# Kernel tuning notes

Hardware: AMD Instinct MI355X
Metric: run time of the kernel (lower is better)

## Reference

```python
import jax, jax.numpy as jnp
import numpy as np
from jax.scipy.special import erf

F = 64          # scalar feature channels (hidden_irreps multiplicity)
S = 9           # spherical harmonics dim for max_ell=2
NB = 8          # num_bessel
RMAX = 5.0
PPOLY = 5       # num_polynomial_cutoff
AVG_NEIGH = 16.0
SIGMA = 1.0     # atomic_multipoles_smearing_width
KE = 1.0        # Coulomb constant (model units)
N = 20000; G = 20; E = 320000; NEL = 10; L = 2; HMLP = 16

def _sph_l2(u):
    # real spherical harmonics up to l=2, e3nn 'component' normalization,
    # with permute_to_e3nn_convention (y, z, x) ordering for l=1
    x, y, z = u[..., 0], u[..., 1], u[..., 2]
    s3 = 1.7320508075688772; s5 = 2.23606797749979; s15 = 3.872983346207417
    return jnp.stack([jnp.ones_like(x),
                      s3 * y, s3 * z, s3 * x,
                      s15 * x * y, s15 * y * z, 0.5 * s5 * (3.0 * z * z - 1.0),
                      s15 * x * z, 0.5 * s15 * (x * x - y * y)], axis=-1)

def _radial(r):
    # Bessel basis with smooth polynomial cutoff (p = PPOLY)
    n = jnp.arange(1, NB + 1, dtype=r.dtype)
    rb = jnp.sqrt(2.0 / RMAX) * jnp.sin(n * jnp.pi * r[:, None] / RMAX) / r[:, None]
    x = r / RMAX
    p = float(PPOLY)
    u = (1.0 - 0.5 * (p + 1.0) * (p + 2.0) * x**PPOLY
         + p * (p + 2.0) * x**(PPOLY + 1) - 0.5 * p * (p + 1.0) * x**(PPOLY + 2))
    u = jnp.where(x < 1.0, u, 0.0)
    return rb * u[:, None]

def setup_inputs() -> dict:
    key = jax.random.key(0)
    ks = jax.random.split(key, 20)
    Ng = N // G
    species = jax.random.randint(ks[0], (N,), 0, NEL)
    node_attrs = jax.nn.one_hot(species, NEL, dtype=jnp.float32)
    positions = jax.random.uniform(ks[1], (N, 3), dtype=jnp.float32) * 10.0
    g = jax.random.randint(ks[2], (E,), 0, G)
    s_loc = jax.random.randint(ks[3], (E,), 0, Ng)
    off = jax.random.randint(ks[4], (E,), 1, Ng)   # avoid self edges
    r_loc = (s_loc + off) % Ng
    edge_index = jnp.stack([g * Ng + s_loc, g * Ng + r_loc], axis=0)
    batch = jnp.repeat(jnp.arange(G), Ng)
    sc = 0.1
    atomic_energies = jax.random.normal(ks[5], (NEL,)) * sc
    embed_w = jax.random.normal(ks[6], (NEL, F)) * sc
    radial_w1 = jax.random.normal(ks[7], (L, NB, 64)) * 0.3
    radial_b1 = jnp.zeros((L, 64), jnp.float32)
    radial_w2 = jax.random.normal(ks[8], (L, 64, F)) * 0.2
    prod_w = jax.random.normal(ks[9], (L, NEL, F)) * 0.3
    readout_w = jax.random.normal(ks[10], (L, F)) * sc
    ro2_w1 = jax.random.normal(ks[11], (F, HMLP)) * 0.2
    ro2_b1 = jnp.zeros((HMLP,), jnp.float32)
    ro2_w2 = jax.random.normal(ks[12], (HMLP, 1)) * 0.2
    charge_w = jax.random.normal(ks[13], (L, F)) * sc
    flux_w = jax.random.normal(ks[14], (L, NB)) * sc
    formal_charges = jax.random.normal(ks[15], (NEL,)) * 0.5
    return dict(node_attrs=node_attrs, positions=positions, edge_index=edge_index,
                batch=batch, num_graphs=G, atomic_energies=atomic_energies,
                embed_w=embed_w, radial_w1=radial_w1, radial_b1=radial_b1,
                radial_w2=radial_w2, prod_w=prod_w, readout_w=readout_w,
                ro2_w1=ro2_w1, ro2_b1=ro2_b1, ro2_w2=ro2_w2,
                charge_w=charge_w, flux_w=flux_w, formal_charges=formal_charges)

def reference(node_attrs, positions, edge_index, batch, num_graphs,
              atomic_energies, embed_w, radial_w1, radial_b1, radial_w2,
              prod_w, readout_w, ro2_w1, ro2_b1, ro2_w2,
              charge_w, flux_w, formal_charges):
    Nn = node_attrs.shape[0]
    Ng = Nn // num_graphs
    snd, rcv = edge_index[0], edge_index[1]
    # atomic reference energies (E0) and node embedding
    node_e0 = node_attrs @ atomic_energies                      # [N]
    e0 = jax.ops.segment_sum(node_e0, batch, num_graphs)        # [G]
    node_scalars = node_attrs @ embed_w                         # [N,F]
    # edge geometry: gather, spherical harmonics, radial embedding
    vec = positions[rcv] - positions[snd]                       # [E,3]
    lengths = jnp.sqrt((vec * vec).sum(-1) + 1e-12)             # [E]
    unit = vec / lengths[:, None]
    edge_attrs = _sph_l2(unit)                                  # [E,S]
    edge_feats = _radial(lengths)                               # [E,NB]
    # formal charges (per-species)
    FQ = node_attrs @ formal_charges                            # [N]
    charge_density = FQ
    flux = jnp.zeros_like(lengths)
    energies = [e0]
    node_e_list = [node_e0]
    nL = radial_w1.shape[0]
    for l in range(nL):
        # interaction: radial MLP -> per-edge TP messages -> scatter sum
        R = jax.nn.silu(edge_feats @ radial_w1[l] + radial_b1[l]) @ radial_w2[l]  # [E,F]
        m = (R * node_scalars[snd])[:, :, None] * edge_attrs[:, None, :]          # [E,F,S]
        agg = jax.ops.segment_sum(m, rcv, Nn) / AVG_NEIGH                         # [N,F,S]
        # equivariant product (correlation-2 flavor) + element-dependent skip
        sk = node_scalars * (node_attrs @ prod_w[l])                              # [N,F]
        feats = agg + agg * agg[:, :, :1]                                         # [N,F,S]
        node_scalars = feats[:, :, 0] + sk                                        # [N,F]
        if l == nL - 1:
            node_energies = (jax.nn.silu(node_scalars @ ro2_w1 + ro2_b1) @ ro2_w2)[:, 0]
        else:
            node_energies = node_scalars @ readout_w[l]
        energies.append(jax.ops.segment_sum(node_energies, batch, num_graphs))
        node_e_list.append(node_energies)
        # long-range source maps: per-node charge + per-edge flux contributions
        charge_density = charge_density + node_scalars @ charge_w[l]
        flux = flux + edge_feats @ flux_w[l]
    contributions = jnp.stack(energies, -1)                     # [G, L+1]
    total_energy = contributions.sum(-1)                        # [G]
    node_energy = jnp.stack(node_e_list, -1).sum(-1)            # [N]
    # polarization: edge-flux dipole + formal-charge dipole
    pol = jax.ops.segment_sum(flux[:, None] * vec, batch[rcv], num_graphs)
    pol = pol + jax.ops.segment_sum(FQ[:, None] * positions, batch, num_graphs)
    # direct (non-PBC) screened Coulomb energy per graph, equal-size graphs
    q = charge_density.reshape(num_graphs, Ng)
    p = positions.reshape(num_graphs, Ng, 3)
    d = p[:, :, None, :] - p[:, None, :, :]
    r = jnp.sqrt((d * d).sum(-1) + 1e-12)
    kern = erf(r / (2.0 * SIGMA)) / r * (1.0 - jnp.eye(Ng, dtype=r.dtype))
    e_el = 0.5 * KE * jnp.einsum('gi,gij,gj->g', q, kern, q)
    total_energy = total_energy + e_el
    total_charge = jax.ops.segment_sum(charge_density, batch, num_graphs)
    return total_energy, node_energy, contributions, pol, total_charge
```

## Files before the change

kernel.cpp:

```cpp
#include <hip/hip_runtime.h>
#include <math.h>

#define NEL 10
#define FD 64
#define NBES 8
#define GG 20
#define HML 16
#define EGB 1280
#define TKNOT 2048
#define TROWS 2049
#define TBBLK 1025

__device__ __forceinline__ float wred(float v) {
    #pragma unroll
    for (int off = 32; off > 0; off >>= 1) v += __shfl_down(v, off, 64);
    return v;
}

__device__ __forceinline__ float silu(float h) {
    return h / (1.f + __expf(-h));
}

__device__ __forceinline__ int xcd_swizzle(int bid, int nb) {
    int q = nb >> 3, r = nb & 7;
    int x = bid & 7, i = bid >> 3;
    return (x < r ? x * (q + 1) : r * (q + 1) + (x - r) * q) + i;
}

__global__ __launch_bounds__(256) void hist_k(
    const int* __restrict__ eidx, int* __restrict__ cnt, int E_)
{
    int e = blockIdx.x * 256 + threadIdx.x;
    atomicAdd(&cnt[eidx[E_ + e]], 1);
}

__global__ __launch_bounds__(1024) void scan_k(
    const int* __restrict__ cnt, int* __restrict__ cur, int N_)
{
    int t = threadIdx.x;
    __shared__ int wtot[16];
    int lane = t & 63, wid = t >> 6;
    int base = t * 20;
    int c[20]; int s = 0;
    bool full = (base + 20 <= N_);
    if (full) {
        #pragma unroll
        for (int i = 0; i < 5; ++i) {
            int4 v4 = *(const int4*)&cnt[base + i * 4];
            c[i*4+0] = v4.x; c[i*4+1] = v4.y; c[i*4+2] = v4.z; c[i*4+3] = v4.w;
        }
        #pragma unroll
        for (int i = 0; i < 20; ++i) s += c[i];
    } else {
        #pragma unroll
        for (int i = 0; i < 20; ++i) { int idx = base + i; c[i] = (idx < N_) ? cnt[idx] : 0; s += c[i]; }
    }
    int v = s;
    #pragma unroll
    for (int off = 1; off < 64; off <<= 1) {
        int u = __shfl_up(v, off, 64);
        if (lane >= off) v += u;
    }
    if (lane == 63) wtot[wid] = v;
    __syncthreads();
    if (wid == 0 && lane < 16) {
        int wv = wtot[lane];
        #pragma unroll
        for (int off = 1; off < 16; off <<= 1) {
            int u = __shfl_up(wv, off, 64);
            if (lane >= off) wv += u;
        }
        wtot[lane] = wv;
    }
    __syncthreads();
    int ex = (wid > 0 ? wtot[wid - 1] : 0) + (v - s);
    if (full) {
        int o[20];
        #pragma unroll
        for (int i = 0; i < 20; ++i) { o[i] = ex; ex += c[i]; }
        #pragma unroll
        for (int i = 0; i < 5; ++i)
            *(int4*)&cur[base + i * 4] = make_int4(o[i*4+0], o[i*4+1], o[i*4+2], o[i*4+3]);
    } else {
        #pragma unroll
        for (int i = 0; i < 20; ++i) {
            int idx = base + i;
            if (idx < N_) { cur[idx] = ex; ex += c[i]; }
        }
    }
}

__global__ __launch_bounds__(256) void setup_geom_k(
    const float* __restrict__ pos, const int* __restrict__ eidx,
    const float* __restrict__ flux_w, int* __restrict__ cur,
    uint2* __restrict__ recs, float* __restrict__ polpart,
    const float* __restrict__ attrs, const float* __restrict__ ae,
    const float* __restrict__ fc, const float* __restrict__ embed_w,
    int* __restrict__ spec, float* __restrict__ q, float* __restrict__ out,
    float* __restrict__ scal,
    const float* __restrict__ w1, const float* __restrict__ b1,
    const float* __restrict__ w2, float* __restrict__ tab,
    int N_, int E_, int ng)
{
    int bid = blockIdx.x, t = threadIdx.x;
    const float PI = 3.14159265358979323846f;
    if (bid < EGB) {
        __shared__ float lpol[GG * 3];
        for (int i = t; i < GG * 3; i += 256) lpol[i] = 0.f;
        __syncthreads();
        int e = bid * 256 + t;
        if (e < E_) {
            float fw[NBES];
            #pragma unroll
            for (int i = 0; i < NBES; ++i) fw[i] = flux_w[i] + flux_w[NBES + i];
            unsigned int magic = (unsigned int)(0xFFFFFFFFull / (unsigned int)ng) + 1u;
            int s = eidx[e], r = eidx[E_ + e];
            float dx = pos[(size_t)r*3+0] - pos[(size_t)s*3+0];
            float dy = pos[(size_t)r*3+1] - pos[(size_t)s*3+1];
            float dz = pos[(size_t)r*3+2] - pos[(size_t)s*3+2];
            float len = sqrtf(dx*dx + dy*dy + dz*dz + 1e-12f);
            float x = len * 0.2f;
            float u = 0.f;
            if (x < 1.f) {
                float x2 = x * x;
                float x5 = x2 * x2 * x;
                u = 1.f - 21.f * x5 + 35.f * x5 * x - 15.f * x5 * x2;
            }
            float pref = 0.6324555320336759f / len * u;
            float theta = PI * x;
            float s1, c1;
            __sincosf(theta, &s1, &c1);
            float c2 = 2.f * c1;
            float sp_ = 0.f, sn = s1;
            float flux = 0.f;
            #pragma unroll
            for (int i = 0; i < NBES; ++i) {
                flux += pref * sn * fw[i];
                float n1 = c2 * sn - sp_; sp_ = sn; sn = n1;
            }
            int p = atomicAdd(&cur[r], 1);
            recs[p] = make_uint2((unsigned int)s | ((unsigned int)r << 16),
                                 __float_as_uint(len));
            int g = (int)__umulhi((unsigned int)r, magic);
            atomicAdd(&lpol[g*3+0], flux * dx);
            atomicAdd(&lpol[g*3+1], flux * dy);
            atomicAdd(&lpol[g*3+2], flux * dz);
        }
        __syncthreads();
        for (int i = t; i < GG * 3; i += 256) polpart[bid * (GG * 3) + i] = lpol[i];
    } else if (bid < EGB + TBBLK) {
        if (bid == EGB && t < GG) out[t] = 0.f;
        int widg = (bid - EGB) * 4 + (t >> 6);
        if (widg < 2 * TROWS) {
            int l = widg / TROWS;
            int kk = widg - l * TROWS;
            int f = t & 63;
            float len = fmaxf((float)kk * (5.f / (float)TKNOT), 1e-6f);
            float x = len * 0.2f;
            float u = 0.f;
            if (x < 1.f) {
                float x2 = x * x;
                float x5 = x2 * x2 * x;
                u = 1.f - 21.f * x5 + 35.f * x5 * x - 15.f * x5 * x2;
            }
            float pref = 0.6324555320336759f / len * u;
            float theta = PI * x;
            float s1, c1;
            __sincosf(theta, &s1, &c1);
            float c2 = 2.f * c1;
            float sp_ = 0.f, sn = s1;
            float ef[NBES];
            #pragma unroll
            for (int i = 0; i < NBES; ++i) {
                ef[i] = pref * sn;
                float n1 = c2 * sn - sp_; sp_ = sn; sn = n1;
            }
            float h = b1[l * FD + f];
            #pragma unroll
            for (int j = 0; j < NBES; ++j)
                h = fmaf(ef[j], w1[l * 512 + j * 64 + f], h);
            h = silu(h);
            float o = 0.f;
            #pragma unroll
            for (int m = 0; m < 64; ++m)
                o = fmaf(__shfl(h, m, 64), w2[(size_t)l * 4096 + m * 64 + f], o);
            float* tbase = tab + (size_t)l * TKNOT * 64 * 2;
            if (kk < TKNOT) tbase[((size_t)kk * 64 + f) * 2 + 0] = o;
            if (kk > 0)     tbase[((size_t)(kk - 1) * 64 + f) * 2 + 1] = o;
        }
    } else {
        int idx = (bid - (EGB + TBBLK)) * 256 + t;
        int lane = t & 63;
        int n = idx >> 6;
        bool pred = (lane < NEL) && (attrs[(size_t)n * NEL + lane] > 0.5f);
        unsigned long long m = __ballot(pred);
        int sp = (int)__builtin_ctzll(m);
        scal[idx] = embed_w[sp * FD + lane];
        if (lane == 0) { spec[n] = sp; q[n] = fc[sp]; out[GG + n] = ae[sp]; }
    }
}

__global__ __launch_bounds__(256, 4) void edge_node_k(
    const uint2* __restrict__ recs, const float* __restrict__ tab,
    const int* __restrict__ cur,
    const float* __restrict__ scal_in, float* __restrict__ scal_out,
    const int* __restrict__ spec, const float* __restrict__ prod_w,
    const float* __restrict__ readout_w, const float* __restrict__ ro2_w1,
    const float* __restrict__ ro2_b1, const float* __restrict__ ro2_w2,
    const float* __restrict__ charge_w, float* __restrict__ q,
    float* __restrict__ out_nodeE, float* __restrict__ nEpart,
    int layer, int last, int N_)
{
    __shared__ float vsh[4][FD];
    int t = threadIdx.x, w = t >> 6, lane = t & 63;
    int xb = xcd_swizzle(blockIdx.x, gridDim.x);
    int rr = xb * 4 + w;
    int e0 = (rr == 0) ? 0 : cur[rr - 1];
    int e1 = cur[rr];
    const float* tb = tab + (size_t)layer * TKNOT * 64 * 2;

    float run = 0.f;

    for (int base = e0; base < e1; base += 64) {
        int nn = e1 - base; if (nn > 64) nn = 64;
        uint2 rec;
        if (base + lane < e1) rec = recs[base + lane];
        else rec = make_uint2(0u, 0u);
        float ln = __uint_as_float(rec.y);
        float ttf = ln * ((float)TKNOT / 5.f);
        int k0 = (int)ttf; k0 = max(0, min(k0, TKNOT - 1));
        float frl = fminf(fmaxf(ttf - (float)k0, 0.f), 1.f);
        int offl = k0 * 128;

        #pragma unroll 1
        for (int sub = 0; sub < 4 && sub * 16 < nn; ++sub) {
            int sb = sub * 16;
            unsigned int idv[16]; int offk[16]; float frk[16];
            #pragma unroll
            for (int k = 0; k < 16; ++k) {
                int pp = sb + k;
                idv[k] = __builtin_amdgcn_readlane(rec.x, pp);
                offk[k] = __builtin_amdgcn_readlane(offl, pp);
                frk[k] = __uint_as_float((unsigned int)__builtin_amdgcn_readlane(
                             __float_as_uint(frl), pp));
            }
            float2 rab[16]; float sw[16];
            #pragma unroll
            for (int k = 0; k < 16; ++k) {
                rab[k] = *(const float2*)&tb[(size_t)offk[k] + lane * 2];
                sw[k]  = scal_in[(size_t)(idv[k] & 0xffffu) * FD + lane];
            }
            #pragma unroll
            for (int k = 0; k < 16; ++k) {
                float R = fmaf(frk[k], rab[k].y - rab[k].x, rab[k].x);
                run += ((sb + k) < nn) ? R * sw[k] : 0.f;
            }
        }
    }

    float a = run * 0.0625f;
    int sp = spec[rr];
    size_t idx = (size_t)rr * FD + lane;
    float v = a + a * a + scal_in[idx] * prod_w[(layer * NEL + sp) * FD + lane];
    if (!last) scal_out[idx] = v;
    float ne;
    if (!last) {
        ne = wred(v * readout_w[layer * FD + lane]);
    } else {
        vsh[w][lane] = v;
        int l16 = lane & 15, qq = lane >> 4;
        float hp = 0.f;
        #pragma unroll
        for (int ff = 0; ff < 16; ++ff) {
            int fidx = qq * 16 + ff;
            hp += vsh[w][fidx] * ro2_w1[fidx * HML + l16];
        }
        hp += __shfl_down(hp, 32, 64);
        hp += __shfl_down(hp, 16, 64);
        float h = 0.f;
        if (lane < HML) h = silu(ro2_b1[lane] + hp) * ro2_w2[lane];
        ne = wred(h);
    }
    float qs = wred(v * charge_w[layer * FD + lane]);
    if (lane == 0) {
        out_nodeE[rr] += ne;
        q[rr] += qs;
        nEpart[(size_t)layer * N_ + rr] = ne;
    }
}

__global__ __launch_bounds__(256) void coulomb_final_k(
    const float* __restrict__ q, const float* __restrict__ pos,
    const int* __restrict__ spec, const float* __restrict__ ae,
    const float* __restrict__ fc, const float* __restrict__ nEpart,
    const float* __restrict__ polpart, float* __restrict__ out,
    int N_, int ng)
{
    __shared__ float sh[260];
    int vb = blockIdx.x;
    int g = vb / 137, rem = vb % 137;
    int t = threadIdx.x, lane = t & 63, w = t >> 6;

    if (rem < 136) {
        int a = 0, r2 = rem;
        while (r2 >= 16 - a) { r2 -= 16 - a; ++a; }
        int b = a + r2;
        const float* qg = q + (size_t)g * ng;
        const float* pg = pos + (size_t)g * ng * 3;
        float* qs_ = sh; float* jx = sh + 64; float* jy = sh + 128; float* jz = sh + 192;
        if (t < 64) {
            int j = b * 64 + t;
            bool ok = j < ng;
            qs_[t] = ok ? qg[j] : 0.f;
            jx[t] = ok ? pg[(size_t)j*3+0] : 0.f;
            jy[t] = ok ? pg[(size_t)j*3+1] : 0.f;
            jz[t] = ok ? pg[(size_t)j*3+2] : 0.f;
        }
        __syncthreads();
        int i = a * 64 + lane;
        float accu = 0.f;
        if (i < ng) {
            float qi = qg[i];
            float xi = pg[(size_t)i*3+0], yi = pg[(size_t)i*3+1], zi = pg[(size_t)i*3+2];
            #pragma unroll 4
            for (int k = 0; k < 16; ++k) {
                int jj = w * 16 + k;
                int j = b * 64 + jj;
                float dx = xi - jx[jj], dy = yi - jy[jj], dz = zi - jz[jj];
                float d2 = dx*dx + dy*dy + dz*dz + 1e-12f;
                float rinv = __frsqrt_rn(d2);
                float r = d2 * rinv;
                float x = 0.5f * r;
                float tt = __frcp_rn(1.f + 0.3275911f * x);
                float poly = ((((1.061405429f*tt - 1.453152027f)*tt + 1.421413741f)*tt
                               - 0.284496736f)*tt + 0.254829592f)*tt;
                float erfv = 1.f - poly * __expf(-x * x);
                float kern = (j == i) ? 0.f : erfv * rinv;
                accu += qi * qs_[jj] * kern;
            }
        }
        accu = wred(accu);
        if (lane == 0) sh[256 + w] = accu;
        __syncthreads();
        if (t == 0) {
            float s = sh[256] + sh[257] + sh[258] + sh[259];
            atomicAdd(&out[g], (a == b) ? 0.5f * s : s);
        }
    } else {
        float se0 = 0.f, sq = 0.f, p0 = 0.f, p1 = 0.f, p2 = 0.f, s0 = 0.f, s1 = 0.f;
        for (int n = g * ng + t; n < (g + 1) * ng; n += 256) {
            int sp = spec[n];
            float fq = fc[sp];
            se0 += ae[sp];
            sq += q[n];
            p0 += fq * pos[(size_t)n*3+0];
            p1 += fq * pos[(size_t)n*3+1];
            p2 += fq * pos[(size_t)n*3+2];
            s0 += nEpart[n];
            s1 += nEpart[(size_t)N_ + n];
        }
        for (int b = t; b < EGB; b += 256) {
            p0 += polpart[b * (GG * 3) + g * 3 + 0];
            p1 += polpart[b * (GG * 3) + g * 3 + 1];
            p2 += polpart[b * (GG * 3) + g * 3 + 2];
        }
        float vals[7] = {se0, s0, s1, sq, p0, p1, p2};
        float* red = sh;
        #pragma unroll
        for (int k = 0; k < 7; ++k) {
            float r = wred(vals[k]);
            if (lane == 0) red[w * 8 + k] = r;
        }
        __syncthreads();
        if (t < 7) sh[64 + t] = red[t] + red[8 + t] + red[16 + t] + red[24 + t];
        __syncthreads();
        if (t == 0) {
            float a0 = sh[64], a1 = sh[65], a2 = sh[66];
            atomicAdd(&out[g], a0 + a1 + a2);
            float* contrib = out + GG + N_;
            contrib[g*3+0] = a0; contrib[g*3+1] = a1; contrib[g*3+2] = a2;
            float* pol = contrib + GG * 3;
            pol[g*3+0] = sh[68]; pol[g*3+1] = sh[69]; pol[g*3+2] = sh[70];
            float* qt = pol + GG * 3;
            qt[g] = sh[67];
        }
    }
}

extern "C" void kernel_launch(void* const* d_in, const int* in_sizes, int n_in,
                              void* d_out, int out_size, void* d_ws, size_t ws_size,
                              hipStream_t stream)
{
    const float* node_attrs      = (const float*)d_in[0];
    const float* positions       = (const float*)d_in[1];
    const int*   edge_index      = (const int*)d_in[2];
    const float* atomic_energies = (const float*)d_in[5];
    const float* embed_w         = (const float*)d_in[6];
    const float* radial_w1       = (const float*)d_in[7];
    const float* radial_b1       = (const float*)d_in[8];
    const float* radial_w2       = (const float*)d_in[9];
    const float* prod_w          = (const float*)d_in[10];
    const float* readout_w       = (const float*)d_in[11];
    const float* ro2_w1          = (const float*)d_in[12];
    const float* ro2_b1          = (const float*)d_in[13];
    const float* ro2_w2          = (const float*)d_in[14];
    const float* charge_w        = (const float*)d_in[15];
    const float* flux_w          = (const float*)d_in[16];
    const float* formal_charges  = (const float*)d_in[17];

    int N = in_sizes[0] / NEL;
    int E = in_sizes[2] / 2;
    int ng = N / GG;

    float* ws      = (float*)d_ws;
    float* scal_a  = ws;
    float* scal_b  = scal_a + (size_t)N * FD;
    int*   cnt     = (int*)(scal_b + (size_t)N * FD);
    int*   cur     = cnt + N;
    uint2* recs    = (uint2*)(cur + N);
    float* q       = (float*)(recs + E);
    int*   spec    = (int*)(q + N);
    float* nEpart  = (float*)(spec + N);
    float* polpart = nEpart + 2 * (size_t)N;
    float* tab     = polpart + EGB * (GG * 3);

    float* out = (float*)d_out;
    float* out_nodeE = out + GG;

    hipMemsetAsync(cnt, 0, (size_t)N * sizeof(int), stream);

    hist_k<<<E / 256, 256, 0, stream>>>(edge_index, cnt, E);
    scan_k<<<1, 1024, 0, stream>>>(cnt, cur, N);
    setup_geom_k<<<EGB + TBBLK + (N * FD) / 256, 256, 0, stream>>>(
        positions, edge_index, flux_w, cur, recs, polpart,
        node_attrs, atomic_energies, formal_charges, embed_w,
        spec, q, out, scal_a, radial_w1, radial_b1, radial_w2, tab, N, E, ng);

    edge_node_k<<<N / 4, 256, 0, stream>>>(
        recs, tab, cur, scal_a, scal_b, spec, prod_w, readout_w,
        ro2_w1, ro2_b1, ro2_w2, charge_w, q, out_nodeE, nEpart, 0, 0, N);
    edge_node_k<<<N / 4, 256, 0, stream>>>(
        recs, tab, cur, scal_b, scal_a, spec, prod_w, readout_w,
        ro2_w1, ro2_b1, ro2_w2, charge_w, q, out_nodeE, nEpart, 1, 1, N);

    coulomb_final_k<<<GG * 137, 256, 0, stream>>>(
        q, positions, spec, atomic_energies, formal_charges,
        nEpart, polpart, out, N, ng);
}
```

Measured before the change: 227.8 us.

## Fuse histogram with table build and node setup into one prep kernel

Merges the edge-receiver histogram into the kernel that builds the radial lookup table and initializes node embeddings, so the table build runs before the scan instead of after it. The edge geometry pass, which needs the scanned offsets, becomes its own kernel. Node embedding init now uses 16 lanes per node with float4 loads and stores instead of 64 scalar lanes. This shortens the serialized critical path around the single-block scan and cuts node-init threads, with the same number of launches.

```diff
diff --git a/kernel.cpp b/kernel.cpp
--- a/kernel.cpp
+++ b/kernel.cpp
@@ -7,6 +7,7 @@
 #define GG 20
 #define HML 16
 #define EGB 1280
+#define HB  1250
 #define TKNOT 2048
 #define TROWS 2049
 #define TBBLK 1025
@@ -27,130 +28,23 @@
     return (x < r ? x * (q + 1) : r * (q + 1) + (x - r) * q) + i;
 }
 
-__global__ __launch_bounds__(256) void hist_k(
-    const int* __restrict__ eidx, int* __restrict__ cnt, int E_)
-{
-    int e = blockIdx.x * 256 + threadIdx.x;
-    atomicAdd(&cnt[eidx[E_ + e]], 1);
-}
-
-__global__ __launch_bounds__(1024) void scan_k(
-    const int* __restrict__ cnt, int* __restrict__ cur, int N_)
-{
-    int t = threadIdx.x;
-    __shared__ int wtot[16];
-    int lane = t & 63, wid = t >> 6;
-    int base = t * 20;
-    int c[20]; int s = 0;
-    bool full = (base + 20 <= N_);
-    if (full) {
-        #pragma unroll
-        for (int i = 0; i < 5; ++i) {
-            int4 v4 = *(const int4*)&cnt[base + i * 4];
-            c[i*4+0] = v4.x; c[i*4+1] = v4.y; c[i*4+2] = v4.z; c[i*4+3] = v4.w;
-        }
-        #pragma unroll
-        for (int i = 0; i < 20; ++i) s += c[i];
-    } else {
-        #pragma unroll
-        for (int i = 0; i < 20; ++i) { int idx = base + i; c[i] = (idx < N_) ? cnt[idx] : 0; s += c[i]; }
-    }
-    int v = s;
-    #pragma unroll
-    for (int off = 1; off < 64; off <<= 1) {
-        int u = __shfl_up(v, off, 64);
-        if (lane >= off) v += u;
-    }
-    if (lane == 63) wtot[wid] = v;
-    __syncthreads();
-    if (wid == 0 && lane < 16) {
-        int wv = wtot[lane];
-        #pragma unroll
-        for (int off = 1; off < 16; off <<= 1) {
-            int u = __shfl_up(wv, off, 64);
-            if (lane >= off) wv += u;
-        }
-        wtot[lane] = wv;
-    }
-    __syncthreads();
-    int ex = (wid > 0 ? wtot[wid - 1] : 0) + (v - s);
-    if (full) {
-        int o[20];
-        #pragma unroll
-        for (int i = 0; i < 20; ++i) { o[i] = ex; ex += c[i]; }
-        #pragma unroll
-        for (int i = 0; i < 5; ++i)
-            *(int4*)&cur[base + i * 4] = make_int4(o[i*4+0], o[i*4+1], o[i*4+2], o[i*4+3]);
-    } else {
-        #pragma unroll
-        for (int i = 0; i < 20; ++i) {
-            int idx = base + i;
-            if (idx < N_) { cur[idx] = ex; ex += c[i]; }
-        }
-    }
-}
-
-__global__ __launch_bounds__(256) void setup_geom_k(
-    const float* __restrict__ pos, const int* __restrict__ eidx,
-    const float* __restrict__ flux_w, int* __restrict__ cur,
-    uint2* __restrict__ recs, float* __restrict__ polpart,
+__global__ __launch_bounds__(256) void prep_k(
+    const int* __restrict__ eidx, int* __restrict__ cnt,
+    const float* __restrict__ w1, const float* __restrict__ b1,
+    const float* __restrict__ w2, float* __restrict__ tab,
     const float* __restrict__ attrs, const float* __restrict__ ae,
     const float* __restrict__ fc, const float* __restrict__ embed_w,
     int* __restrict__ spec, float* __restrict__ q, float* __restrict__ out,
-    float* __restrict__ scal,
-    const float* __restrict__ w1, const float* __restrict__ b1,
-    const float* __restrict__ w2, float* __restrict__ tab,
-    int N_, int E_, int ng)
+    float* __restrict__ scal, int N_, int E_)
 {
     int bid = blockIdx.x, t = threadIdx.x;
     const float PI = 3.14159265358979323846f;
-    if (bid < EGB) {
-        __shared__ float lpol[GG * 3];
-        for (int i = t; i < GG * 3; i += 256) lpol[i] = 0.f;
-        __syncthreads();
+    if (bid < HB) {
         int e = bid * 256 + t;
-        if (e < E_) {
-            float fw[NBES];
-            #pragma unroll
-            for (int i = 0; i < NBES; ++i) fw[i] = flux_w[i] + flux_w[NBES + i];
-            unsigned int magic = (unsigned int)(0xFFFFFFFFull / (unsigned int)ng) + 1u;
-            int s = eidx[e], r = eidx[E_ + e];
-            float dx = pos[(size_t)r*3+0] - pos[(size_t)s*3+0];
-            float dy = pos[(size_t)r*3+1] - pos[(size_t)s*3+1];
-            float dz = pos[(size_t)r*3+2] - pos[(size_t)s*3+2];
-            float len = sqrtf(dx*dx + dy*dy + dz*dz + 1e-12f);
-            float x = len * 0.2f;
-            float u = 0.f;
-            if (x < 1.f) {
-                float x2 = x * x;
-                float x5 = x2 * x2 * x;
-                u = 1.f - 21.f * x5 + 35.f * x5 * x - 15.f * x5 * x2;
-            }
-            float pref = 0.6324555320336759f / len * u;
-            float theta = PI * x;
-            float s1, c1;
-            __sincosf(theta, &s1, &c1);
-            float c2 = 2.f * c1;
-            float sp_ = 0.f, sn = s1;
-            float flux = 0.f;
-            #pragma unroll
-            for (int i = 0; i < NBES; ++i) {
-                flux += pref * sn * fw[i];
-                float n1 = c2 * sn - sp_; sp_ = sn; sn = n1;
-            }
-            int p = atomicAdd(&cur[r], 1);
-            recs[p] = make_uint2((unsigned int)s | ((unsigned int)r << 16),
-                                 __float_as_uint(len));
-            int g = (int)__umulhi((unsigned int)r, magic);
-            atomicAdd(&lpol[g*3+0], flux * dx);
-            atomicAdd(&lpol[g*3+1], flux * dy);
-            atomicAdd(&lpol[g*3+2], flux * dz);
-        }
-        __syncthreads();
-        for (int i = t; i < GG * 3; i += 256) polpart[bid * (GG * 3) + i] = lpol[i];
-    } else if (bid < EGB + TBBLK) {
-        if (bid == EGB && t < GG) out[t] = 0.f;
-        int widg = (bid - EGB) * 4 + (t >> 6);
+        if (e < E_) atomicAdd(&cnt[eidx[E_ + e]], 1);
+    } else if (bid < HB + TBBLK) {
+        if (bid == HB && t < GG) out[t] = 0.f;
+        int widg = (bid - HB) * 4 + (t >> 6);
         if (widg < 2 * TROWS) {
             int l = widg / TROWS;
             int kk = widg - l * TROWS;
@@ -189,15 +83,126 @@
             if (kk > 0)     tbase[((size_t)(kk - 1) * 64 + f) * 2 + 1] = o;
         }
     } else {
-        int idx = (bid - (EGB + TBBLK)) * 256 + t;
-        int lane = t & 63;
-        int n = idx >> 6;
-        bool pred = (lane < NEL) && (attrs[(size_t)n * NEL + lane] > 0.5f);
+        int idx = (bid - (HB + TBBLK)) * 256 + t;
+        int n = idx >> 4;
+        int li = idx & 15;
+        bool pred = (li < NEL) && (attrs[(size_t)n * NEL + li] > 0.5f);
         unsigned long long m = __ballot(pred);
-        int sp = (int)__builtin_ctzll(m);
-        scal[idx] = embed_w[sp * FD + lane];
-        if (lane == 0) { spec[n] = sp; q[n] = fc[sp]; out[GG + n] = ae[sp]; }
-    }
+        int gi = (t & 63) >> 4;
+        int sp = (int)__builtin_ctzll((m >> (16 * gi)) & 0xFFFFull);
+        float4 ev = *(const float4*)&embed_w[sp * FD + li * 4];
+        *(float4*)&scal[(size_t)n * FD + li * 4] = ev;
+        if (li == 0) { spec[n] = sp; q[n] = fc[sp]; out[GG + n] = ae[sp]; }
+    }
+}
+
+__global__ __launch_bounds__(1024) void scan_k(
+    const int* __restrict__ cnt, int* __restrict__ cur, int N_)
+{
+    int t = threadIdx.x;
+    __shared__ int wtot[16];
+    int lane = t & 63, wid = t >> 6;
+    int base = t * 20;
+    int c[20]; int s = 0;
+    bool full = (base + 20 <= N_);
+    if (full) {
+        #pragma unroll
+        for (int i = 0; i < 5; ++i) {
+            int4 v4 = *(const int4*)&cnt[base + i * 4];
+            c[i*4+0] = v4.x; c[i*4+1] = v4.y; c[i*4+2] = v4.z; c[i*4+3] = v4.w;
+        }
+        #pragma unroll
+        for (int i = 0; i < 20; ++i) s += c[i];
+    } else {
+        #pragma unroll
+        for (int i = 0; i < 20; ++i) { int idx = base + i; c[i] = (idx < N_) ? cnt[idx] : 0; s += c[i]; }
+    }
+    int v = s;
+    #pragma unroll
+    for (int off = 1; off < 64; off <<= 1) {
+        int u = __shfl_up(v, off, 64);
+        if (lane >= off) v += u;
+    }
+    if (lane == 63) wtot[wid] = v;
+    __syncthreads();
+    if (wid == 0 && lane < 16) {
+        int wv = wtot[lane];
+        #pragma unroll
+        for (int off = 1; off < 16; off <<= 1) {
+            int u = __shfl_up(wv, off, 64);
+            if (lane >= off) wv += u;
+        }
+        wtot[lane] = wv;
+    }
+    __syncthreads();
+    int ex = (wid > 0 ? wtot[wid - 1] : 0) + (v - s);
+    if (full) {
+        int o[20];
+        #pragma unroll
+        for (int i = 0; i < 20; ++i) { o[i] = ex; ex += c[i]; }
+        #pragma unroll
+        for (int i = 0; i < 5; ++i)
+            *(int4*)&cur[base + i * 4] = make_int4(o[i*4+0], o[i*4+1], o[i*4+2], o[i*4+3]);
+    } else {
+        #pragma unroll
+        for (int i = 0; i < 20; ++i) {
+            int idx = base + i;
+            if (idx < N_) { cur[idx] = ex; ex += c[i]; }
+        }
+    }
+}
+
+__global__ __launch_bounds__(256) void geom_k(
+    const float* __restrict__ pos, const int* __restrict__ eidx,
+    const float* __restrict__ flux_w, int* __restrict__ cur,
+    uint2* __restrict__ recs, float* __restrict__ polpart,
+    int E_, int ng)
+{
+    __shared__ float lpol[GG * 3];
+    int bid = blockIdx.x, t = threadIdx.x;
+    const float PI = 3.14159265358979323846f;
+    for (int i = t; i < GG * 3; i += 256) lpol[i] = 0.f;
+    __syncthreads();
+    int e = bid * 256 + t;
+    if (e < E_) {
+        float fw[NBES];
+        #pragma unroll
+        for (int i = 0; i < NBES; ++i) fw[i] = flux_w[i] + flux_w[NBES + i];
+        unsigned int magic = (unsigned int)(0xFFFFFFFFull / (unsigned int)ng) + 1u;
+        int s = eidx[e], r = eidx[E_ + e];
+        float dx = pos[(size_t)r*3+0] - pos[(size_t)s*3+0];
+        float dy = pos[(size_t)r*3+1] - pos[(size_t)s*3+1];
+        float dz = pos[(size_t)r*3+2] - pos[(size_t)s*3+2];
+        float len = sqrtf(dx*dx + dy*dy + dz*dz + 1e-12f);
+        float x = len * 0.2f;
+        float u = 0.f;
+        if (x < 1.f) {
+            float x2 = x * x;
+            float x5 = x2 * x2 * x;
+            u = 1.f - 21.f * x5 + 35.f * x5 * x - 15.f * x5 * x2;
+        }
+        float pref = 0.6324555320336759f / len * u;
+        float theta = PI * x;
+        float s1, c1;
+        __sincosf(theta, &s1, &c1);
+        float c2 = 2.f * c1;
+        float sp_ = 0.f, sn = s1;
+        float flux = 0.f;
+        #pragma unroll
+        for (int i = 0; i < NBES; ++i) {
+            flux += pref * sn * fw[i];
+            float n1 = c2 * sn - sp_; sp_ = sn; sn = n1;
+        }
+        int p = atomicAdd(&cur[r], 1);
+        recs[p] = make_uint2((unsigned int)s | ((unsigned int)r << 16),
+                             __float_as_uint(len));
+        int g = (int)__umulhi((unsigned int)r, magic);
+        atomicAdd(&lpol[g*3+0], flux * dx);
+        atomicAdd(&lpol[g*3+1], flux * dy);
+        atomicAdd(&lpol[g*3+2], flux * dz);
+    }
+    __syncthreads();
+    for (int i = t; i < GG * 3; i += 256) polpart[bid * (GG * 3) + i] = lpol[i];
 }
 
 __global__ __launch_bounds__(256, 4) void edge_node_k(
@@ -429,12 +434,13 @@
 
     hipMemsetAsync(cnt, 0, (size_t)N * sizeof(int), stream);
 
-    hist_k<<<E / 256, 256, 0, stream>>>(edge_index, cnt, E);
+    prep_k<<<HB + TBBLK + (N * FD) / 1024, 256, 0, stream>>>(
+        edge_index, cnt, radial_w1, radial_b1, radial_w2, tab,
+        node_attrs, atomic_energies, formal_charges, embed_w,
+        spec, q, out, scal_a, N, E);
     scan_k<<<1, 1024, 0, stream>>>(cnt, cur, N);
-    setup_geom_k<<<EGB + TBBLK + (N * FD) / 256, 256, 0, stream>>>(
-        positions, edge_index, flux_w, cur, recs, polpart,
-        node_attrs, atomic_energies, formal_charges, embed_w,
-        spec, q, out, scal_a, radial_w1, radial_b1, radial_w2, tab, N, E, ng);
+    geom_k<<<EGB, 256, 0, stream>>>(
+        positions, edge_index, flux_w, cur, recs, polpart, E, ng);
 
     edge_node_k<<<N / 4, 256, 0, stream>>>(
         recs, tab, cur, scal_a, scal_b, spec, prod_w, readout_w,
```

New measurement: 231.8 us. Within noise of the previous version (+1.8%).
